# Optimization experiments

Measured on AMD Instinct MI355X. Metric: run time of the kernel, lower is better.

The kernel has to match this reference:

```python
import jax, jax.numpy as jnp
import numpy as np
import math

LENGTH_SEQUENSE = 300  # hardcoded scale in the original module (NOT d_k)


def setup_inputs() -> dict:
    key = jax.random.key(0)
    k1, k2 = jax.random.split(key)
    B, S, D_in, D_out = 256, 300, 512, 512
    x = jax.random.normal(k1, (B, S, D_in), dtype=jnp.float32)
    weight_matrix = jax.random.normal(k2, (3, D_in, D_out), dtype=jnp.float32) * 0.02
    return {"x": x, "weight_matrix": weight_matrix}


def reference(x, weight_matrix):
    # Q/K/V projections: [B,S,D_in] @ [D_in,D_out] -> [B,S,D_out]
    query = jnp.einsum('bsd,de->bse', x, weight_matrix[0])
    key_ = jnp.einsum('bsd,de->bse', x, weight_matrix[1])
    value = jnp.einsum('bsd,de->bse', x, weight_matrix[2])
    # scores: [B,S,S]; faithful to original: scaled by sqrt(length_sequense)=sqrt(300)
    scores = jnp.einsum('bqe,bke->bqk', query, key_) / math.sqrt(LENGTH_SEQUENSE)
    attn = jax.nn.softmax(scores, axis=-1)
    # output: [B,S,D_out]
    return jnp.einsum('bqk,bke->bqe', attn, value)
```

## Files before the change

### kernel.cpp

```cpp
#include <hip/hip_runtime.h>
#include <hip/hip_bf16.h>
#include <math.h>

typedef __attribute__((ext_vector_type(8))) __bf16 bf16x8;
typedef __attribute__((ext_vector_type(8))) short  s16x8;
typedef __attribute__((ext_vector_type(4))) float  f32x4;
union SB8 { s16x8 s; bf16x8 b; };

__device__ __forceinline__ unsigned short f2bf(float f) {
  unsigned int u = __builtin_bit_cast(unsigned int, f);
  u = u + 0x7FFFu + ((u >> 16) & 1u);
  return (unsigned short)(u >> 16);
}

__device__ __forceinline__ void glds16(const void* g, void* l) {
  __builtin_amdgcn_global_load_lds((const __attribute__((address_space(1))) void*)g,
                                   (__attribute__((address_space(3))) void*)l, 16, 0, 0);
}

#define B_  256
#define S_  300
#define D_  512
#define SP  320
#define M_  76800
#define XS  544

__global__ __launch_bounds__(256) void k_cvt_x(const float* __restrict__ x,
                                               unsigned short* __restrict__ xb, int n8) {
  int i = blockIdx.x * blockDim.x + threadIdx.x;
  int stride = gridDim.x * blockDim.x;
  for (; i < n8; i += stride) {
    const float4* p = (const float4*)(x + (size_t)i * 8);
    float4 a = p[0], b = p[1];
    union { unsigned short u[8]; s16x8 v; } o;
    o.u[0]=f2bf(a.x); o.u[1]=f2bf(a.y); o.u[2]=f2bf(a.z); o.u[3]=f2bf(a.w);
    o.u[4]=f2bf(b.x); o.u[5]=f2bf(b.y); o.u[6]=f2bf(b.z); o.u[7]=f2bf(b.w);
    int row = i >> 6, c8 = i & 63;
    *(s16x8*)(xb + (size_t)row * XS + c8 * 8) = o.v;
  }
}

__global__ __launch_bounds__(256) void k_wt2(const float* __restrict__ w,
                                             unsigned short* __restrict__ wb01,
                                             unsigned short* __restrict__ wtv) {
  int i = blockIdx.x * 256 + threadIdx.x;
  int p = i >> 18;
  int r = i & 262143;
  unsigned short v = f2bf(w[i]);
  if (p < 2) {
    wb01[p * 262144 + r] = v;
  } else {
    int k = r >> 9, n = r & 511;
    wtv[n * 512 + k] = v;
  }
}

__global__ __launch_bounds__(256) void k_G(const unsigned short* __restrict__ wb01,
                                           unsigned short* __restrict__ gjd) {
  __shared__ short As[2][128 * 64];
  __shared__ short Bs[2][128 * 64];
  const unsigned short* wa = wb01 + 262144;
  const unsigned short* wb = wb01;
  int bid = blockIdx.x;
  int mt = bid >> 2, n0 = (bid & 3) * 128;
  int rowBase = mt * 128;

  int tid = threadIdx.x, lane = tid & 63, wid = tid >> 6;
  int wr = wid >> 1, wc = wid & 1;
  int sr = lane >> 3;
  int ssg = ((lane & 7) ^ sr) * 8;
  int fr = lane & 15;
  int g  = lane >> 4;
  f32x4 acc[4][4] = {};

  for (int c = wid * 4; c < wid * 4 + 4; ++c) {
    glds16(wa + (size_t)(rowBase + c * 8 + sr) * 512 + ssg, &As[0][c * 512 + lane * 8]);
    glds16(wb + (size_t)(n0 + c * 8 + sr) * 512 + ssg, &Bs[0][c * 512 + lane * 8]);
  }
  __syncthreads();

  for (int t = 0; t < 8; ++t) {
    int cur = t & 1;
    if (t < 7) {
      int k0n = (t + 1) * 64;
      for (int c = wid * 4; c < wid * 4 + 4; ++c) {
        glds16(wa + (size_t)(rowBase + c * 8 + sr) * 512 + k0n + ssg,
               &As[cur ^ 1][c * 512 + lane * 8]);
        glds16(wb + (size_t)(n0 + c * 8 + sr) * 512 + k0n + ssg,
               &Bs[cur ^ 1][c * 512 + lane * 8]);
      }
    }
    SB8 aF[4][2], bF[4][2];
#pragma unroll
    for (int m = 0; m < 4; ++m) {
      int row = wr * 64 + m * 16 + fr;
#pragma unroll
      for (int kk = 0; kk < 2; ++kk) {
        int sl = ((kk << 2) + g) ^ (fr & 7);
        aF[m][kk].s = *(const s16x8*)&As[cur][row * 64 + sl * 8];
      }
    }
#pragma unroll
    for (int n = 0; n < 4; ++n) {
      int row = wc * 64 + n * 16 + fr;
#pragma unroll
      for (int kk = 0; kk < 2; ++kk) {
        int sl = ((kk << 2) + g) ^ (fr & 7);
        bF[n][kk].s = *(const s16x8*)&Bs[cur][row * 64 + sl * 8];
      }
    }
#pragma unroll
    for (int kk = 0; kk < 2; ++kk)
#pragma unroll
      for (int m = 0; m < 4; ++m)
#pragma unroll
        for (int n = 0; n < 4; ++n)
          acc[m][n] = __builtin_amdgcn_mfma_f32_16x16x32_bf16(aF[m][kk].b, bF[n][kk].b,
                                                              acc[m][n], 0, 0, 0);
    __syncthreads();
  }

  int fq = lane >> 4;
#pragma unroll
  for (int m = 0; m < 4; ++m)
#pragma unroll
    for (int n = 0; n < 4; ++n) {
      int row = rowBase + wr * 64 + m * 16 + fq * 4;
      int col = n0 + wc * 64 + n * 16 + fr;
      unsigned short* o = gjd + (size_t)row * 512 + col;
#pragma unroll
      for (int jj = 0; jj < 4; ++jj)
        o[(size_t)jj * 512] = f2bf(acc[m][n][jj]);
    }
}

__global__ __launch_bounds__(256) void k_projT(const unsigned short* __restrict__ xb,
                                               const unsigned short* __restrict__ gjd,
                                               unsigned short* __restrict__ Tout) {
  __shared__ short As[2][128 * 64];
  __shared__ short Bs[2][128 * 64];
  int bid = blockIdx.x;
  int xc = bid & 7, j = bid >> 3;
  int mt = xc + 8 * (j >> 2);
  int n0 = (j & 3) * 128;
  int rowBase = mt * 128;

  int tid = threadIdx.x, lane = tid & 63, wid = tid >> 6;
  int wr = wid >> 1, wc = wid & 1;
  int sr = lane >> 3;
  int ssg = ((lane & 7) ^ sr) * 8;
  int fr = lane & 15;
  int g  = lane >> 4;
  f32x4 acc[4][4] = {};

  for (int c = wid * 4; c < wid * 4 + 4; ++c) {
    glds16(xb + (size_t)(rowBase + c * 8 + sr) * XS + ssg, &As[0][c * 512 + lane * 8]);
    glds16(gjd + (size_t)(n0 + c * 8 + sr) * 512 + ssg, &Bs[0][c * 512 + lane * 8]);
  }
  __syncthreads();

  for (int t = 0; t < 8; ++t) {
    int cur = t & 1;
    if (t < 7) {
      int k0n = (t + 1) * 64;
      for (int c = wid * 4; c < wid * 4 + 4; ++c) {
        glds16(xb + (size_t)(rowBase + c * 8 + sr) * XS + k0n + ssg,
               &As[cur ^ 1][c * 512 + lane * 8]);
        glds16(gjd + (size_t)(n0 + c * 8 + sr) * 512 + k0n + ssg,
               &Bs[cur ^ 1][c * 512 + lane * 8]);
      }
    }
    SB8 aF[4][2], bF[4][2];
#pragma unroll
    for (int m = 0; m < 4; ++m) {
      int row = wr * 64 + m * 16 + fr;
#pragma unroll
      for (int kk = 0; kk < 2; ++kk) {
        int sl = ((kk << 2) + g) ^ (fr & 7);
        aF[m][kk].s = *(const s16x8*)&As[cur][row * 64 + sl * 8];
      }
    }
#pragma unroll
    for (int n = 0; n < 4; ++n) {
      int row = wc * 64 + n * 16 + fr;
#pragma unroll
      for (int kk = 0; kk < 2; ++kk) {
        int sl = ((kk << 2) + g) ^ (fr & 7);
        bF[n][kk].s = *(const s16x8*)&Bs[cur][row * 64 + sl * 8];
      }
    }
#pragma unroll
    for (int kk = 0; kk < 2; ++kk)
#pragma unroll
      for (int m = 0; m < 4; ++m)
#pragma unroll
        for (int n = 0; n < 4; ++n)
          acc[m][n] = __builtin_amdgcn_mfma_f32_16x16x32_bf16(aF[m][kk].b, bF[n][kk].b,
                                                              acc[m][n], 0, 0, 0);
    __syncthreads();
  }

  int fq = lane >> 4;
#pragma unroll
  for (int m = 0; m < 4; ++m)
#pragma unroll
    for (int n = 0; n < 4; ++n) {
      int row = rowBase + wr * 64 + m * 16 + fq * 4;
      int col = n0 + wc * 64 + n * 16 + fr;
      unsigned short* o = Tout + (size_t)row * XS + col;
#pragma unroll
      for (int jj = 0; jj < 4; ++jj)
        o[(size_t)jj * XS] = f2bf(acc[m][n][jj]);
    }
}

__global__ __launch_bounds__(256) void k_projV(const unsigned short* __restrict__ xb,
                                               const unsigned short* __restrict__ wtv,
                                               unsigned short* __restrict__ vt) {
  __shared__ short As[2][128 * 64];
  __shared__ short Bs[2][128 * 64];
  int bid = blockIdx.x;
  int xc = bid & 7, j = bid >> 3;
  int mt = xc + 8 * (j >> 2);
  int n0 = (j & 3) * 128;
  int rowBase = mt * 128;
  const unsigned short* wp = wtv;

  int tid = threadIdx.x, lane = tid & 63, wid = tid >> 6;
  int wr = wid >> 1, wc = wid & 1;
  int sr = lane >> 3;
  int ssg = ((lane & 7) ^ sr) * 8;
  int fr = lane & 15;
  int g  = lane >> 4;
  f32x4 acc[4][4] = {};

  for (int c = wid * 4; c < wid * 4 + 4; ++c) {
    glds16(xb + (size_t)(rowBase + c * 8 + sr) * XS + ssg, &As[0][c * 512 + lane * 8]);
    glds16(wp + (size_t)(n0 + c * 8 + sr) * 512 + ssg, &Bs[0][c * 512 + lane * 8]);
  }
  __syncthreads();

  for (int t = 0; t < 8; ++t) {
    int cur = t & 1;
    if (t < 7) {
      int k0n = (t + 1) * 64;
      for (int c = wid * 4; c < wid * 4 + 4; ++c) {
        glds16(xb + (size_t)(rowBase + c * 8 + sr) * XS + k0n + ssg,
               &As[cur ^ 1][c * 512 + lane * 8]);
        glds16(wp + (size_t)(n0 + c * 8 + sr) * 512 + k0n + ssg,
               &Bs[cur ^ 1][c * 512 + lane * 8]);
      }
    }
    SB8 aF[4][2], bF[4][2];
#pragma unroll
    for (int m = 0; m < 4; ++m) {
      int row = wr * 64 + m * 16 + fr;
#pragma unroll
      for (int kk = 0; kk < 2; ++kk) {
        int sl = ((kk << 2) + g) ^ (fr & 7);
        aF[m][kk].s = *(const s16x8*)&As[cur][row * 64 + sl * 8];
      }
    }
#pragma unroll
    for (int n = 0; n < 4; ++n) {
      int row = wc * 64 + n * 16 + fr;
#pragma unroll
      for (int kk = 0; kk < 2; ++kk) {
        int sl = ((kk << 2) + g) ^ (fr & 7);
        bF[n][kk].s = *(const s16x8*)&Bs[cur][row * 64 + sl * 8];
      }
    }
#pragma unroll
    for (int kk = 0; kk < 2; ++kk)
#pragma unroll
      for (int m = 0; m < 4; ++m)
#pragma unroll
        for (int n = 0; n < 4; ++n)
          acc[m][n] = __builtin_amdgcn_mfma_f32_16x16x32_bf16(aF[m][kk].b, bF[n][kk].b,
                                                              acc[m][n], 0, 0, 0);
    __syncthreads();
  }

  int fq = lane >> 4;
  short* T2 = &As[0][0];
#pragma unroll
  for (int m = 0; m < 4; ++m) {
    int s0 = wr * 64 + m * 16 + fq * 4;
#pragma unroll
    for (int n16 = 0; n16 < 4; ++n16) {
      int c = wc * 64 + n16 * 16 + fr;
      int idx = c * 128 + (s0 ^ ((c & 7) << 4));
      union { unsigned short u[4]; uint2 v; } w;
#pragma unroll
      for (int jj = 0; jj < 4; ++jj) w.u[jj] = f2bf(acc[m][n16][jj]);
      *(uint2*)&T2[idx] = w.v;
    }
  }
  __syncthreads();
  for (int i = 0; i < 8; ++i) {
    int u = i * 256 + tid;
    int n = u >> 4, ch = u & 15;
    int idx = n * 128 + ((ch * 8) ^ ((n & 7) << 4));
    s16x8 vv = *(const s16x8*)&T2[idx];
    size_t ncol = (size_t)(n0 + n);
#pragma unroll
    for (int h = 0; h < 2; ++h) {
      int gs = rowBase + ch * 8 + h * 4;
      int bb = (unsigned)gs / 300u;
      int sloc = gs - bb * 300;
      union { unsigned short u[4]; uint2 v; } w;
#pragma unroll
      for (int e = 0; e < 4; ++e) w.u[e] = (unsigned short)vv[h * 4 + e];
      *(uint2*)(vt + (size_t)bb * (512 * SP) + ncol * SP + sloc) = w.v;
    }
  }
}

__global__ __launch_bounds__(256) void k_attn_p(const unsigned short* __restrict__ Q,
                                                const unsigned short* __restrict__ K,
                                                unsigned short* __restrict__ P) {
  __shared__ float S[32 * 320];
  int bid = blockIdx.x;
  int xcd = bid & 7, slot = bid >> 3;
  int b = xcd * 32 + slot / 10;
  int qt = slot % 10;
  int qBase = qt * 32;
  const unsigned short* Qb = Q + (size_t)b * S_ * XS;
  const unsigned short* Kb = K + (size_t)b * S_ * XS;
  unsigned short* Pb = P + (size_t)b * S_ * SP;
  int tid = threadIdx.x, lane = tid & 63, wid = tid >> 6;
  int kg = (lane >> 4) * 8, fr = lane & 15;
  int g = lane >> 4;

  int qr0 = qBase + fr;      if (qr0 > 299) qr0 = 299;
  int qr1 = qBase + 16 + fr; if (qr1 > 299) qr1 = 299;
  const unsigned short* Qr0 = Qb + (size_t)qr0 * XS + kg;
  const unsigned short* Qr1 = Qb + (size_t)qr1 * XS + kg;

  int ntBase = wid * 5;
  const unsigned short* Kr[5];
#pragma unroll
  for (int n = 0; n < 5; ++n) {
    int kr = (ntBase + n) * 16 + fr; if (kr > 299) kr = 299;
    Kr[n] = Kb + (size_t)kr * XS + kg;
  }

  f32x4 acc[2][5] = {};
#pragma unroll
  for (int t = 0; t < 16; ++t) {
    int k0 = t * 32;
    SB8 qF[2], kF[5];
    qF[0].s = *(const s16x8*)(Qr0 + k0);
    qF[1].s = *(const s16x8*)(Qr1 + k0);
#pragma unroll
    for (int n = 0; n < 5; ++n)
      kF[n].s = *(const s16x8*)(Kr[n] + k0);
#pragma unroll
    for (int m = 0; m < 2; ++m)
#pragma unroll
      for (int n = 0; n < 5; ++n)
        acc[m][n] = __builtin_amdgcn_mfma_f32_16x16x32_bf16(qF[m].b, kF[n].b, acc[m][n], 0, 0, 0);
  }

  const float scale = 0.05773502691896258f;
#pragma unroll
  for (int m = 0; m < 2; ++m)
#pragma unroll
    for (int n = 0; n < 5; ++n) {
      int col = (ntBase + n) * 16 + fr;
      int rb = m * 16 + g * 4;
#pragma unroll
      for (int jj = 0; jj < 4; ++jj)
        S[(rb + jj) * 320 + (col ^ (jj << 3))] = acc[m][n][jj] * scale;
    }
  __syncthreads();

  {
    int r = tid >> 3, jj = tid & 7;
    int rx = (r & 3) << 3;
    int c0 = jj * 40;
    int cend = c0 + 40; if (cend > 300) cend = 300;
    float* Sr = &S[r * 320];
    float m0 = -1e30f, m1 = -1e30f, m2 = -1e30f, m3 = -1e30f;
    for (int c = c0; c < cend; c += 4) {
      int cs = c ^ rx;
      m0 = fmaxf(m0, Sr[cs]);     m1 = fmaxf(m1, Sr[cs + 1]);
      m2 = fmaxf(m2, Sr[cs + 2]); m3 = fmaxf(m3, Sr[cs + 3]);
    }
    float mx = fmaxf(fmaxf(m0, m1), fmaxf(m2, m3));
    mx = fmaxf(mx, __shfl_xor(mx, 1));
    mx = fmaxf(mx, __shfl_xor(mx, 2));
    mx = fmaxf(mx, __shfl_xor(mx, 4));
    float s0 = 0.f, s1 = 0.f, s2 = 0.f, s3 = 0.f;
    for (int c = c0; c < cend; c += 4) {
      int cs = c ^ rx;
      float e0 = __expf(Sr[cs] - mx);     Sr[cs] = e0;     s0 += e0;
      float e1 = __expf(Sr[cs + 1] - mx); Sr[cs + 1] = e1; s1 += e1;
      float e2 = __expf(Sr[cs + 2] - mx); Sr[cs + 2] = e2; s2 += e2;
      float e3 = __expf(Sr[cs + 3] - mx); Sr[cs + 3] = e3; s3 += e3;
    }
    float sum = (s0 + s1) + (s2 + s3);
    sum += __shfl_xor(sum, 1);
    sum += __shfl_xor(sum, 2);
    sum += __shfl_xor(sum, 4);
    float inv = 1.0f / sum;
    int qrow = qBase + r;
    if (qrow < 300) {
#pragma unroll
      for (int i = 0; i < 5; ++i) {
        int cb = c0 + i * 8;
        int cbs = cb ^ rx;
        union { unsigned short u[8]; s16x8 v; } o;
#pragma unroll
        for (int e = 0; e < 8; ++e) {
          int cc = cb + e;
          o.u[e] = (cc < 300) ? f2bf(Sr[cbs + e] * inv) : (unsigned short)0;
        }
        *(s16x8*)(Pb + (size_t)qrow * SP + cb) = o.v;
      }
    }
  }
}

__global__ __launch_bounds__(256) void k_pv(const unsigned short* __restrict__ P,
                                            const unsigned short* __restrict__ Vt,
                                            float* __restrict__ O) {
  __shared__ short As[128 * 32];
  __shared__ short Bs[128 * 32];
  int bid = blockIdx.x;
  int xc = bid & 7, j = bid >> 3;
  int b = xc + 8 * (j / 12);
  int tile = j % 12;
  int mt = tile >> 2, n0 = (tile & 3) * 128;
  int rowBase = mt * 128;
  const unsigned short* Pb  = P  + (size_t)b * S_ * SP;
  const unsigned short* Vtb = Vt + (size_t)b * 512 * SP;
  float* Ob = O + (size_t)b * S_ * 512;
  int tid = threadIdx.x, lane = tid & 63, wid = tid >> 6;
  int wr = wid >> 1, wc = wid & 1;
  int sr4 = lane >> 2;
  int ss = ((lane & 3) ^ ((lane >> 3) & 3)) * 8;
  int fr = lane & 15;
  int g = lane >> 4;
  int sl = (g ^ ((fr >> 1) & 3)) * 8;
  f32x4 acc[4][4] = {};

  for (int t = 0; t < 10; ++t) {
    int k0 = t * 32;
    for (int c = wid * 2; c < wid * 2 + 2; ++c) {
      int row = rowBase + c * 16 + sr4; if (row > 299) row = 299;
      glds16(Pb + (size_t)row * SP + k0 + ss, &As[c * 512 + lane * 8]);
    }
    for (int c = wid * 2; c < wid * 2 + 2; ++c)
      glds16(Vtb + (size_t)(n0 + c * 16 + sr4) * SP + k0 + ss,
             &Bs[c * 512 + lane * 8]);
    __syncthreads();
    SB8 aF[4], bF[4];
#pragma unroll
    for (int m = 0; m < 4; ++m) {
      int row = wr * 64 + m * 16 + fr;
      aF[m].s = *(const s16x8*)&As[row * 32 + sl];
    }
#pragma unroll
    for (int n = 0; n < 4; ++n) {
      int row = wc * 64 + n * 16 + fr;
      bF[n].s = *(const s16x8*)&Bs[row * 32 + sl];
    }
#pragma unroll
    for (int m = 0; m < 4; ++m)
#pragma unroll
      for (int n = 0; n < 4; ++n)
        acc[m][n] = __builtin_amdgcn_mfma_f32_16x16x32_bf16(aF[m].b, bF[n].b, acc[m][n], 0, 0, 0);
    __syncthreads();
  }
  int fq = lane >> 4;
#pragma unroll
  for (int m = 0; m < 4; ++m)
#pragma unroll
    for (int n = 0; n < 4; ++n) {
      int col = n0 + wc * 64 + n * 16 + fr;
#pragma unroll
      for (int jj = 0; jj < 4; ++jj) {
        int row = rowBase + wr * 64 + m * 16 + fq * 4 + jj;
        if (row < 300) Ob[(size_t)row * 512 + col] = acc[m][n][jj];
      }
    }
}

extern "C" void kernel_launch(void* const* d_in, const int* in_sizes, int n_in,
                              void* d_out, int out_size, void* d_ws, size_t ws_size,
                              hipStream_t stream) {
  const float* x = (const float*)d_in[0];
  const float* w = (const float*)d_in[1];
  float* out = (float*)d_out;
  char* ws = (char*)d_ws;

  unsigned short* Tq   = (unsigned short*)d_out;
  unsigned short* Vt   = (unsigned short*)(ws);
  unsigned short* xb   = (unsigned short*)(ws + 83886080LL);
  unsigned short* Pp   = (unsigned short*)(ws + 167444480LL);
  unsigned short* wtv  = (unsigned short*)(ws + 216596480LL);
  unsigned short* wb01 = (unsigned short*)(ws + 217120768LL);
  unsigned short* Gjd  = (unsigned short*)(ws + 218169344LL);

  k_cvt_x<<<2048, 256, 0, stream>>>(x, xb, 4915200);
  k_wt2<<<3072, 256, 0, stream>>>(w, wb01, wtv);
  k_G<<<16, 256, 0, stream>>>(wb01, Gjd);
  k_projT<<<2400, 256, 0, stream>>>(xb, Gjd, Tq);
  k_attn_p<<<2560, 256, 0, stream>>>(Tq, xb, Pp);
  k_projV<<<2400, 256, 0, stream>>>(xb, wtv, Vt);
  k_pv<<<3072, 256, 0, stream>>>(Pp, Vt, out);
}
```

Baseline: 365.9 us.

## Fuse softmax-probability and PV matmul into one attention kernel

Merges the softmax kernel and the separate P·V GEMM into one kernel. Unnormalized probabilities stay in shared memory as bf16, and each wave computes a 32x128 output slice straight from V read out of global memory. Normalization is deferred to the epilogue through a per-row inverse sum. This removes the global write and read-back of the P matrix and one launch. The cost is that V fragments are loaded without LDS staging, the block uses more shared memory (lower occupancy), and the Tq buffer moves from the output into the workspace.

```diff
diff --git a/kernel.cpp b/kernel.cpp
--- a/kernel.cpp
+++ b/kernel.cpp
@@ -24,6 +24,7 @@
 #define SP  320
 #define M_  76800
 #define XS  544
+#define PS  328
 
 __global__ __launch_bounds__(256) void k_cvt_x(const float* __restrict__ x,
                                                unsigned short* __restrict__ xb, int n8) {
@@ -316,10 +317,13 @@
   }
 }
 
-__global__ __launch_bounds__(256) void k_attn_p(const unsigned short* __restrict__ Q,
-                                                const unsigned short* __restrict__ K,
-                                                unsigned short* __restrict__ P) {
+__global__ __launch_bounds__(256) void k_attn(const unsigned short* __restrict__ Q,
+                                              const unsigned short* __restrict__ K,
+                                              const unsigned short* __restrict__ Vt,
+                                              float* __restrict__ O) {
   __shared__ float S[32 * 320];
+  __shared__ unsigned short Pb[32 * PS];
+  __shared__ float invS[32];
   int bid = blockIdx.x;
   int xcd = bid & 7, slot = bid >> 3;
   int b = xcd * 32 + slot / 10;
@@ -327,7 +331,8 @@
   int qBase = qt * 32;
   const unsigned short* Qb = Q + (size_t)b * S_ * XS;
   const unsigned short* Kb = K + (size_t)b * S_ * XS;
-  unsigned short* Pb = P + (size_t)b * S_ * SP;
+  const unsigned short* Vb = Vt + (size_t)b * 512 * SP;
+  float* Ob = O + (size_t)b * S_ * 512;
   int tid = threadIdx.x, lane = tid & 63, wid = tid >> 6;
   int kg = (lane >> 4) * 8, fr = lane & 15;
   int g = lane >> 4;
@@ -403,88 +408,57 @@
     sum += __shfl_xor(sum, 1);
     sum += __shfl_xor(sum, 2);
     sum += __shfl_xor(sum, 4);
-    float inv = 1.0f / sum;
-    int qrow = qBase + r;
-    if (qrow < 300) {
-#pragma unroll
-      for (int i = 0; i < 5; ++i) {
-        int cb = c0 + i * 8;
-        int cbs = cb ^ rx;
-        union { unsigned short u[8]; s16x8 v; } o;
-#pragma unroll
-        for (int e = 0; e < 8; ++e) {
-          int cc = cb + e;
-          o.u[e] = (cc < 300) ? f2bf(Sr[cbs + e] * inv) : (unsigned short)0;
+    if (jj == 0) invS[r] = 1.0f / sum;
+#pragma unroll
+    for (int i = 0; i < 5; ++i) {
+      int cb = c0 + i * 8;
+      int cbs = cb ^ rx;
+      union { unsigned short u[8]; s16x8 v; } o;
+#pragma unroll
+      for (int e = 0; e < 8; ++e) {
+        int cc = cb + e;
+        o.u[e] = (cc < 300) ? f2bf(Sr[cbs + e]) : (unsigned short)0;
+      }
+      *(s16x8*)(&Pb[r * PS + cb]) = o.v;
+    }
+  }
+  __syncthreads();
+
+  {
+    int n0w = wid * 128;
+    f32x4 av[2][8] = {};
+#pragma unroll
+    for (int t = 0; t < 10; ++t) {
+      int k0 = t * 32;
+      SB8 aF[2], vF[8];
+      aF[0].s = *(const s16x8*)&Pb[(fr) * PS + k0 + kg];
+      aF[1].s = *(const s16x8*)&Pb[(16 + fr) * PS + k0 + kg];
+#pragma unroll
+      for (int nt = 0; nt < 8; ++nt)
+        vF[nt].s = *(const s16x8*)(Vb + (size_t)(n0w + nt * 16 + fr) * SP + k0 + kg);
+#pragma unroll
+      for (int m = 0; m < 2; ++m)
+#pragma unroll
+        for (int nt = 0; nt < 8; ++nt)
+          av[m][nt] = __builtin_amdgcn_mfma_f32_16x16x32_bf16(aF[m].b, vF[nt].b,
+                                                              av[m][nt], 0, 0, 0);
+    }
+#pragma unroll
+    for (int m = 0; m < 2; ++m)
+#pragma unroll
+      for (int jj = 0; jj < 4; ++jj) {
+        int row = m * 16 + g * 4 + jj;
+        int qrow = qBase + row;
+        if (qrow < 300) {
+          float inv = invS[row];
+#pragma unroll
+          for (int nt = 0; nt < 8; ++nt) {
+            int col = n0w + nt * 16 + fr;
+            Ob[(size_t)qrow * 512 + col] = av[m][nt][jj] * inv;
+          }
         }
-        *(s16x8*)(Pb + (size_t)qrow * SP + cb) = o.v;
-      }
-    }
-  }
-}
-
-__global__ __launch_bounds__(256) void k_pv(const unsigned short* __restrict__ P,
-                                            const unsigned short* __restrict__ Vt,
-                                            float* __restrict__ O) {
-  __shared__ short As[128 * 32];
-  __shared__ short Bs[128 * 32];
-  int bid = blockIdx.x;
-  int xc = bid & 7, j = bid >> 3;
-  int b = xc + 8 * (j / 12);
-  int tile = j % 12;
-  int mt = tile >> 2, n0 = (tile & 3) * 128;
-  int rowBase = mt * 128;
-  const unsigned short* Pb  = P  + (size_t)b * S_ * SP;
-  const unsigned short* Vtb = Vt + (size_t)b * 512 * SP;
-  float* Ob = O + (size_t)b * S_ * 512;
-  int tid = threadIdx.x, lane = tid & 63, wid = tid >> 6;
-  int wr = wid >> 1, wc = wid & 1;
-  int sr4 = lane >> 2;
-  int ss = ((lane & 3) ^ ((lane >> 3) & 3)) * 8;
-  int fr = lane & 15;
-  int g = lane >> 4;
-  int sl = (g ^ ((fr >> 1) & 3)) * 8;
-  f32x4 acc[4][4] = {};
-
-  for (int t = 0; t < 10; ++t) {
-    int k0 = t * 32;
-    for (int c = wid * 2; c < wid * 2 + 2; ++c) {
-      int row = rowBase + c * 16 + sr4; if (row > 299) row = 299;
-      glds16(Pb + (size_t)row * SP + k0 + ss, &As[c * 512 + lane * 8]);
-    }
-    for (int c = wid * 2; c < wid * 2 + 2; ++c)
-      glds16(Vtb + (size_t)(n0 + c * 16 + sr4) * SP + k0 + ss,
-             &Bs[c * 512 + lane * 8]);
-    __syncthreads();
-    SB8 aF[4], bF[4];
-#pragma unroll
-    for (int m = 0; m < 4; ++m) {
-      int row = wr * 64 + m * 16 + fr;
-      aF[m].s = *(const s16x8*)&As[row * 32 + sl];
-    }
-#pragma unroll
-    for (int n = 0; n < 4; ++n) {
-      int row = wc * 64 + n * 16 + fr;
-      bF[n].s = *(const s16x8*)&Bs[row * 32 + sl];
-    }
-#pragma unroll
-    for (int m = 0; m < 4; ++m)
-#pragma unroll
-      for (int n = 0; n < 4; ++n)
-        acc[m][n] = __builtin_amdgcn_mfma_f32_16x16x32_bf16(aF[m].b, bF[n].b, acc[m][n], 0, 0, 0);
-    __syncthreads();
-  }
-  int fq = lane >> 4;
-#pragma unroll
-  for (int m = 0; m < 4; ++m)
-#pragma unroll
-    for (int n = 0; n < 4; ++n) {
-      int col = n0 + wc * 64 + n * 16 + fr;
-#pragma unroll
-      for (int jj = 0; jj < 4; ++jj) {
-        int row = rowBase + wr * 64 + m * 16 + fq * 4 + jj;
-        if (row < 300) Ob[(size_t)row * 512 + col] = acc[m][n][jj];
-      }
-    }
+      }
+  }
 }
 
 extern "C" void kernel_launch(void* const* d_in, const int* in_sizes, int n_in,
@@ -495,19 +469,17 @@
   float* out = (float*)d_out;
   char* ws = (char*)d_ws;
 
-  unsigned short* Tq   = (unsigned short*)d_out;
   unsigned short* Vt   = (unsigned short*)(ws);
   unsigned short* xb   = (unsigned short*)(ws + 83886080LL);
-  unsigned short* Pp   = (unsigned short*)(ws + 167444480LL);
-  unsigned short* wtv  = (unsigned short*)(ws + 216596480LL);
-  unsigned short* wb01 = (unsigned short*)(ws + 217120768LL);
-  unsigned short* Gjd  = (unsigned short*)(ws + 218169344LL);
+  unsigned short* Tq   = (unsigned short*)(ws + 167444480LL);
+  unsigned short* wtv  = (unsigned short*)(ws + 251002880LL);
+  unsigned short* wb01 = (unsigned short*)(ws + 251527168LL);
+  unsigned short* Gjd  = (unsigned short*)(ws + 252575744LL);
 
   k_cvt_x<<<2048, 256, 0, stream>>>(x, xb, 4915200);
   k_wt2<<<3072, 256, 0, stream>>>(w, wb01, wtv);
   k_G<<<16, 256, 0, stream>>>(wb01, Gjd);
+  k_projV<<<2400, 256, 0, stream>>>(xb, wtv, Vt);
   k_projT<<<2400, 256, 0, stream>>>(xb, Gjd, Tq);
-  k_attn_p<<<2560, 256, 0, stream>>>(Tq, xb, Pp);
-  k_projV<<<2400, 256, 0, stream>>>(xb, wtv, Vt);
-  k_pv<<<3072, 256, 0, stream>>>(Pp, Vt, out);
-}
+  k_attn<<<2560, 256, 0, stream>>>(Tq, xb, Vt, out);
+}
```

New measurement: 451.0 us. +23.3%, slower.
